# Performance work log

Measured on AMD Instinct MI355X. Metric: run time of the kernel, lower is better.

The kernel has to match this reference:

```python
import jax, jax.numpy as jnp
import numpy as np

N, E = 100000, 800000   # nodes, edges
H, F = 12, 8            # heads, per-head features
D = H * F               # 96 = num_in_features
LRELU_SLOPE = 0.2
LN_EPS = 1e-6


def setup_inputs() -> dict:
    key = jax.random.key(0)
    k1, k2, k3, k4, k5, k6 = jax.random.split(key, 6)
    x = jax.random.normal(k1, (N, D), dtype=jnp.float32)
    edge_index = jax.random.randint(k2, (2, E), 0, N, dtype=jnp.int64)
    # linear_proj: Linear(D, H*F, bias=False); init std = (D*H*F)**-0.5
    w_proj = jax.random.normal(k3, (D, D), dtype=jnp.float32) * (D * H * F) ** -0.5
    score_src = jax.random.normal(k4, (1, H, F), dtype=jnp.float32) * (H * F) ** -0.5
    score_trg = jax.random.normal(k5, (1, H, F), dtype=jnp.float32) * (H * F) ** -0.5
    ln_weight = jnp.ones((D,), dtype=jnp.float32)
    return {"x": x, "edge_index": edge_index, "w_proj": w_proj,
            "score_src": score_src, "score_trg": score_trg, "ln_weight": ln_weight}


def reference(x, edge_index, w_proj, score_src, score_trg, ln_weight):
    # dropout layers are identity (inference mode)
    src = edge_index[0]
    trg = edge_index[1]
    proj = x.reshape(N, H, F)                        # view, no projection (as in source)
    s_src = jnp.sum(proj * score_src, axis=-1)       # [N, H]
    s_trg = jnp.sum(proj * score_trg, axis=-1)       # [N, H]
    # lift to edges + leaky relu
    scores = s_src[src] + s_trg[trg]                 # [E, H]
    scores = jnp.where(scores >= 0, scores, LRELU_SLOPE * scores)
    # neighborhood-aware (segment) softmax over target nodes
    scores = scores - jnp.max(scores)
    exp_scores = jnp.exp(scores)                     # [E, H]
    denom = jax.ops.segment_sum(exp_scores, trg, num_segments=N)  # [N, H]
    attn = exp_scores / (denom[trg] + 1e-16)         # [E, H]
    # weighted aggregation of lifted source features
    weighted = proj[src] * attn[:, :, None]          # [E, H, F]
    agg = jax.ops.segment_sum(weighted, trg, num_segments=N)      # [N, H, F]
    out = agg.reshape(N, H * F)
    # RMS-style LayerNorm (no mean subtraction, weight only)
    var = jnp.mean(jnp.square(out.astype(jnp.float32)), axis=-1, keepdims=True)
    out = ln_weight * (out * jax.lax.rsqrt(var + LN_EPS))
    out = out @ w_proj.T                             # linear_proj, no bias
    return x + out
```

## Files before the change

kernel.cpp:

```cpp
#include <hip/hip_runtime.h>
#include <math.h>

#define NN 100000
#define EE 800000
#define HH 12
#define FF 8
#define DD 96
#define NBLK_SCAN 98
#define WROW 104

typedef __bf16 bf16x8 __attribute__((ext_vector_type(8)));
typedef float  f32x4  __attribute__((ext_vector_type(4)));

static __device__ __forceinline__ unsigned short f2bf(float f) {
    unsigned u = __builtin_bit_cast(unsigned, f);
    u += 0x7fffu + ((u >> 16) & 1u);
    return (unsigned short)(u >> 16);
}
static __device__ __forceinline__ unsigned packbf(float a, float b) {
    return (unsigned)f2bf(a) | ((unsigned)f2bf(b) << 16);
}

__global__ __launch_bounds__(256) void k_scores(
    const float* __restrict__ x, const float* __restrict__ wsrc,
    const float* __restrict__ wtrg, float* __restrict__ s_src,
    float* __restrict__ s_trg, int* __restrict__ counts)
{
    int tid = blockIdx.x * 256 + threadIdx.x;
    if (tid < NN) counts[tid] = 0;
    if (tid >= NN * HH) return;
    int h = tid % HH;
    int n = tid / HH;
    const float4* xp = (const float4*)(x + (size_t)n * DD + h * FF);
    float4 a = xp[0], b = xp[1];
    const float4* s4 = (const float4*)(wsrc + h * FF);
    const float4* t4 = (const float4*)(wtrg + h * FF);
    float4 sa = s4[0], sb = s4[1];
    float4 ta = t4[0], tb = t4[1];
    s_src[tid] = a.x*sa.x + a.y*sa.y + a.z*sa.z + a.w*sa.w
               + b.x*sb.x + b.y*sb.y + b.z*sb.z + b.w*sb.w;
    s_trg[tid] = a.x*ta.x + a.y*ta.y + a.z*ta.z + a.w*ta.w
               + b.x*tb.x + b.y*tb.y + b.z*tb.z + b.w*tb.w;
}

__global__ __launch_bounds__(256) void k_hist(const int* __restrict__ ei,
                                              int* __restrict__ counts)
{
    int e = blockIdx.x * 256 + threadIdx.x;
    if (e >= EE) return;
    int t = ei[EE + e];
    atomicAdd(&counts[t], 1);
}

__global__ __launch_bounds__(256) void k_chunks(const int* __restrict__ counts,
                                                int* __restrict__ chunks)
{
    __shared__ int sd[256];
    int t = threadIdx.x;
    int base = blockIdx.x * 1024 + t * 4;
    int s = 0;
    #pragma unroll
    for (int j = 0; j < 4; ++j) {
        int i = base + j;
        s += (i < NN) ? counts[i] : 0;
    }
    sd[t] = s;
    __syncthreads();
    for (int off = 128; off > 0; off >>= 1) {
        if (t < off) sd[t] += sd[t + off];
        __syncthreads();
    }
    if (t == 0) chunks[blockIdx.x] = sd[0];
}

__global__ __launch_bounds__(256) void k_scan(const int* __restrict__ counts,
                                              const int* __restrict__ chunks,
                                              int* __restrict__ offsets,
                                              int* __restrict__ cursor)
{
    __shared__ int sc[128];
    __shared__ int sd[256];
    int t = threadIdx.x;
    if (t < 128) sc[t] = (t < NBLK_SCAN) ? chunks[t] : 0;
    __syncthreads();
    for (int off = 1; off < 128; off <<= 1) {
        int u = (t < 128 && t >= off) ? sc[t - off] : 0;
        __syncthreads();
        if (t < 128) sc[t] += u;
        __syncthreads();
    }
    int bof = (blockIdx.x == 0) ? 0 : sc[blockIdx.x - 1];

    int base = blockIdx.x * 1024 + t * 4;
    int c[4];
    int s = 0;
    #pragma unroll
    for (int j = 0; j < 4; ++j) {
        int i = base + j;
        c[j] = (i < NN) ? counts[i] : 0;
        s += c[j];
    }
    sd[t] = s;
    __syncthreads();
    for (int off = 1; off < 256; off <<= 1) {
        int u = (t >= off) ? sd[t - off] : 0;
        __syncthreads();
        sd[t] += u;
        __syncthreads();
    }
    int run = bof + ((t == 0) ? 0 : sd[t - 1]);
    #pragma unroll
    for (int j = 0; j < 4; ++j) {
        int i = base + j;
        if (i < NN) { offsets[i] = run; cursor[i] = run; }
        run += c[j];
    }
}

__global__ __launch_bounds__(256) void k_scatter(const int* __restrict__ ei,
                                                 int* __restrict__ cursor,
                                                 int* __restrict__ esrc)
{
    int e = blockIdx.x * 256 + threadIdx.x;
    if (e >= EE) return;
    int s = ei[e];
    int t = ei[EE + e];
    int pos = atomicAdd(&cursor[t], 1);
    esrc[pos] = s;
}

__global__ __launch_bounds__(768) void k_aggout(
    const float* __restrict__ x, const float* __restrict__ s_src,
    const float* __restrict__ s_trg, const int* __restrict__ offsets,
    const int* __restrict__ counts, const int* __restrict__ esrc,
    const float* __restrict__ lnw, const float* __restrict__ w,
    float* __restrict__ out)
{
    __shared__ char lds_raw[(96 + 64) * WROW * 2];
    __shared__ float nsq[64];
    unsigned short* wl = (unsigned short*)lds_raw;
    unsigned short* yl = ((unsigned short*)lds_raw) + 96 * WROW;
    int t    = threadIdx.x;
    int tile = blockIdx.x * 64;
    int nrem = NN - tile;

    if (t < 64) nsq[t] = 0.f;
    #pragma unroll
    for (int i = 0; i < 3; ++i) {
        int lin = t * 4 + i * 3072;
        int r = lin / 96, c = lin - (lin / 96) * 96;
        float4 v = *(const float4*)(w + lin);
        unsigned* p = (unsigned*)(wl + r * WROW + c);
        p[0] = packbf(v.x, v.y); p[1] = packbf(v.z, v.w);
    }
    __syncthreads();

    {
        int ln = t / HH;
        int h  = t - ln * HH;
        int n  = tile + ln;
        bool valid = (n < NN);
        float st = 0.f; int beg = 0, cnt = 0;
        if (valid) {
            st  = s_trg[n * HH + h];
            beg = offsets[n];
            cnt = counts[n];
        }
        float denom = 0.f;
        float4 aa = {0.f, 0.f, 0.f, 0.f};
        float4 ab = {0.f, 0.f, 0.f, 0.f};
        int s_cur = (cnt > 0) ? esrc[beg] : 0;
        for (int k = 0; k < cnt; ++k) {
            int s_nxt = (k + 1 < cnt) ? esrc[beg + k + 1] : 0;
            float sc = s_src[s_cur * HH + h] + st;
            sc = (sc >= 0.f) ? sc : 0.2f * sc;
            float ex = __expf(sc);
            denom += ex;
            const float4* xp = (const float4*)(x + (size_t)s_cur * DD + h * FF);
            float4 a = xp[0], b = xp[1];
            aa.x += a.x * ex; aa.y += a.y * ex; aa.z += a.z * ex; aa.w += a.w * ex;
            ab.x += b.x * ex; ab.y += b.y * ex; ab.z += b.z * ex; ab.w += b.w * ex;
            s_cur = s_nxt;
        }
        float inv = 1.f / (denom + 1e-16f);
        float yp[8];
        yp[0] = aa.x * inv; yp[1] = aa.y * inv; yp[2] = aa.z * inv; yp[3] = aa.w * inv;
        yp[4] = ab.x * inv; yp[5] = ab.y * inv; yp[6] = ab.z * inv; yp[7] = ab.w * inv;
        float ss = 0.f;
        #pragma unroll
        for (int j = 0; j < 8; ++j) ss += yp[j] * yp[j];
        atomicAdd(&nsq[ln], ss);
        __syncthreads();
        float scale = rsqrtf(nsq[ln] * (1.f / 96.f) + 1e-6f);
        const float4* lw = (const float4*)(lnw + h * FF);
        float4 w1 = lw[0], w2 = lw[1];
        unsigned* yo = (unsigned*)(yl + ln * WROW + h * FF);
        yo[0] = packbf(yp[0] * scale * w1.x, yp[1] * scale * w1.y);
        yo[1] = packbf(yp[2] * scale * w1.z, yp[3] * scale * w1.w);
        yo[2] = packbf(yp[4] * scale * w2.x, yp[5] * scale * w2.y);
        yo[3] = packbf(yp[6] * scale * w2.z, yp[7] * scale * w2.w);
    }
    __syncthreads();

    int wv = t >> 6;
    int l  = t & 63;
    int tt0 = wv * 2;
    int rt  = tt0 / 6;
    int ct0 = tt0 - rt * 6;
    int kchunk = (l >> 4) * 8;
    int arow = rt * 16 + (l & 15);
    f32x4 acc0 = {}, acc1 = {};
    #pragma unroll
    for (int s = 0; s < 3; ++s) {
        bf16x8 af = *(const bf16x8*)(yl + arow * WROW + s * 32 + kchunk);
        bf16x8 b0 = *(const bf16x8*)(wl + ((ct0 + 0) * 16 + (l & 15)) * WROW + s * 32 + kchunk);
        bf16x8 b1 = *(const bf16x8*)(wl + ((ct0 + 1) * 16 + (l & 15)) * WROW + s * 32 + kchunk);
        acc0 = __builtin_amdgcn_mfma_f32_16x16x32_bf16(af, b0, acc0, 0, 0, 0);
        acc1 = __builtin_amdgcn_mfma_f32_16x16x32_bf16(af, b1, acc1, 0, 0, 0);
    }
    __syncthreads();

    float* fb = (float*)lds_raw;
    {
        int row = rt * 16 + (l >> 4) * 4;
        int col = ct0 * 16 + (l & 15);
        #pragma unroll
        for (int r = 0; r < 4; ++r) {
            fb[(row + r) * 97 + col]      = acc0[r];
            fb[(row + r) * 97 + col + 16] = acc1[r];
        }
    }
    __syncthreads();
    #pragma unroll
    for (int i = 0; i < 2; ++i) {
        int lin = t * 4 + i * 3072;
        int r = lin / 96, c = lin - (lin / 96) * 96;
        if (r < nrem) {
            float4 xv = *(const float4*)(x + (size_t)tile * DD + lin);
            float4 o;
            o.x = xv.x + fb[r * 97 + c + 0];
            o.y = xv.y + fb[r * 97 + c + 1];
            o.z = xv.z + fb[r * 97 + c + 2];
            o.w = xv.w + fb[r * 97 + c + 3];
            *(float4*)(out + (size_t)tile * DD + lin) = o;
        }
    }
}

extern "C" void kernel_launch(void* const* d_in, const int* in_sizes, int n_in,
                              void* d_out, int out_size, void* d_ws, size_t ws_size,
                              hipStream_t stream)
{
    const float* x    = (const float*)d_in[0];
    const int*   ei   = (const int*)d_in[1];
    const float* wprj = (const float*)d_in[2];
    const float* wsrc = (const float*)d_in[3];
    const float* wtrg = (const float*)d_in[4];
    const float* lnw  = (const float*)d_in[5];
    float* out = (float*)d_out;

    float* s_src  = (float*)d_ws;
    float* s_trg  = s_src + NN * HH;
    int*   counts = (int*)(s_trg + NN * HH);
    int*   offs   = counts + NN;
    int*   cursor = offs + NN;
    int*   chunks = cursor + NN;
    int*   esrc   = chunks + 128;

    k_scores<<<(NN * HH + 255) / 256, 256, 0, stream>>>(x, wsrc, wtrg, s_src, s_trg, counts);
    k_hist<<<(EE + 255) / 256, 256, 0, stream>>>(ei, counts);
    k_chunks<<<NBLK_SCAN, 256, 0, stream>>>(counts, chunks);
    k_scan<<<NBLK_SCAN, 256, 0, stream>>>(counts, chunks, offs, cursor);
    k_scatter<<<(EE + 255) / 256, 256, 0, stream>>>(ei, cursor, esrc);
    k_aggout<<<(NN + 63) / 64, 768, 0, stream>>>(x, s_src, s_trg, offs, counts, esrc, lnw, wprj, out);
}
```

Measured before the change: 269.6 us.

## Gather bf16 copy of node features and replace scatter atomics with histogram ranks

k_scores now also writes a bf16 copy of x, and the edge-aggregation loop gathers 16-byte bf16 rows instead of 32-byte fp32 rows, halving gather traffic in the dominant kernel. The histogram kernel records each edge's atomic return value as a rank, so the scatter kernel computes positions as offset plus rank without a second round of atomics, and the cursor array goes away. The cost is an extra 19 MB bf16 write plus a rank array, and reduced precision in the aggregated features.

```diff
diff --git a/kernel.cpp b/kernel.cpp
--- a/kernel.cpp
+++ b/kernel.cpp
@@ -20,11 +20,18 @@
 static __device__ __forceinline__ unsigned packbf(float a, float b) {
     return (unsigned)f2bf(a) | ((unsigned)f2bf(b) << 16);
 }
+static __device__ __forceinline__ float bflo(unsigned u) {
+    return __builtin_bit_cast(float, u << 16);
+}
+static __device__ __forceinline__ float bfhi(unsigned u) {
+    return __builtin_bit_cast(float, u & 0xffff0000u);
+}
 
 __global__ __launch_bounds__(256) void k_scores(
     const float* __restrict__ x, const float* __restrict__ wsrc,
     const float* __restrict__ wtrg, float* __restrict__ s_src,
-    float* __restrict__ s_trg, int* __restrict__ counts)
+    float* __restrict__ s_trg, int* __restrict__ counts,
+    unsigned short* __restrict__ xb)
 {
     int tid = blockIdx.x * 256 + threadIdx.x;
     if (tid < NN) counts[tid] = 0;
@@ -33,6 +40,9 @@
     int n = tid / HH;
     const float4* xp = (const float4*)(x + (size_t)n * DD + h * FF);
     float4 a = xp[0], b = xp[1];
+    unsigned* xo = (unsigned*)(xb + (size_t)n * DD + h * FF);
+    xo[0] = packbf(a.x, a.y); xo[1] = packbf(a.z, a.w);
+    xo[2] = packbf(b.x, b.y); xo[3] = packbf(b.z, b.w);
     const float4* s4 = (const float4*)(wsrc + h * FF);
     const float4* t4 = (const float4*)(wtrg + h * FF);
     float4 sa = s4[0], sb = s4[1];
@@ -44,12 +54,13 @@
 }
 
 __global__ __launch_bounds__(256) void k_hist(const int* __restrict__ ei,
-                                              int* __restrict__ counts)
+                                              int* __restrict__ counts,
+                                              int* __restrict__ rank)
 {
     int e = blockIdx.x * 256 + threadIdx.x;
     if (e >= EE) return;
     int t = ei[EE + e];
-    atomicAdd(&counts[t], 1);
+    rank[e] = atomicAdd(&counts[t], 1);
 }
 
 __global__ __launch_bounds__(256) void k_chunks(const int* __restrict__ counts,
@@ -75,8 +86,7 @@
 
 __global__ __launch_bounds__(256) void k_scan(const int* __restrict__ counts,
                                               const int* __restrict__ chunks,
-                                              int* __restrict__ offsets,
-                                              int* __restrict__ cursor)
+                                              int* __restrict__ offsets)
 {
     __shared__ int sc[128];
     __shared__ int sd[256];
@@ -112,29 +122,29 @@
     #pragma unroll
     for (int j = 0; j < 4; ++j) {
         int i = base + j;
-        if (i < NN) { offsets[i] = run; cursor[i] = run; }
+        if (i < NN) offsets[i] = run;
         run += c[j];
     }
 }
 
 __global__ __launch_bounds__(256) void k_scatter(const int* __restrict__ ei,
-                                                 int* __restrict__ cursor,
+                                                 const int* __restrict__ offsets,
+                                                 const int* __restrict__ rank,
                                                  int* __restrict__ esrc)
 {
     int e = blockIdx.x * 256 + threadIdx.x;
     if (e >= EE) return;
     int s = ei[e];
     int t = ei[EE + e];
-    int pos = atomicAdd(&cursor[t], 1);
-    esrc[pos] = s;
+    esrc[offsets[t] + rank[e]] = s;
 }
 
 __global__ __launch_bounds__(768) void k_aggout(
-    const float* __restrict__ x, const float* __restrict__ s_src,
-    const float* __restrict__ s_trg, const int* __restrict__ offsets,
-    const int* __restrict__ counts, const int* __restrict__ esrc,
-    const float* __restrict__ lnw, const float* __restrict__ w,
-    float* __restrict__ out)
+    const float* __restrict__ x, const unsigned short* __restrict__ xb,
+    const float* __restrict__ s_src, const float* __restrict__ s_trg,
+    const int* __restrict__ offsets, const int* __restrict__ counts,
+    const int* __restrict__ esrc, const float* __restrict__ lnw,
+    const float* __restrict__ w, float* __restrict__ out)
 {
     __shared__ char lds_raw[(96 + 64) * WROW * 2];
     __shared__ float nsq[64];
@@ -167,8 +177,7 @@
             cnt = counts[n];
         }
         float denom = 0.f;
-        float4 aa = {0.f, 0.f, 0.f, 0.f};
-        float4 ab = {0.f, 0.f, 0.f, 0.f};
+        float acc[8] = {0.f, 0.f, 0.f, 0.f, 0.f, 0.f, 0.f, 0.f};
         int s_cur = (cnt > 0) ? esrc[beg] : 0;
         for (int k = 0; k < cnt; ++k) {
             int s_nxt = (k + 1 < cnt) ? esrc[beg + k + 1] : 0;
@@ -176,16 +185,17 @@
             sc = (sc >= 0.f) ? sc : 0.2f * sc;
             float ex = __expf(sc);
             denom += ex;
-            const float4* xp = (const float4*)(x + (size_t)s_cur * DD + h * FF);
-            float4 a = xp[0], b = xp[1];
-            aa.x += a.x * ex; aa.y += a.y * ex; aa.z += a.z * ex; aa.w += a.w * ex;
-            ab.x += b.x * ex; ab.y += b.y * ex; ab.z += b.z * ex; ab.w += b.w * ex;
+            uint4 q = *(const uint4*)(xb + (size_t)s_cur * DD + h * FF);
+            acc[0] += bflo(q.x) * ex; acc[1] += bfhi(q.x) * ex;
+            acc[2] += bflo(q.y) * ex; acc[3] += bfhi(q.y) * ex;
+            acc[4] += bflo(q.z) * ex; acc[5] += bfhi(q.z) * ex;
+            acc[6] += bflo(q.w) * ex; acc[7] += bfhi(q.w) * ex;
             s_cur = s_nxt;
         }
         float inv = 1.f / (denom + 1e-16f);
         float yp[8];
-        yp[0] = aa.x * inv; yp[1] = aa.y * inv; yp[2] = aa.z * inv; yp[3] = aa.w * inv;
-        yp[4] = ab.x * inv; yp[5] = ab.y * inv; yp[6] = ab.z * inv; yp[7] = ab.w * inv;
+        #pragma unroll
+        for (int j = 0; j < 8; ++j) yp[j] = acc[j] * inv;
         float ss = 0.f;
         #pragma unroll
         for (int j = 0; j < 8; ++j) ss += yp[j] * yp[j];
@@ -263,14 +273,15 @@
     float* s_trg  = s_src + NN * HH;
     int*   counts = (int*)(s_trg + NN * HH);
     int*   offs   = counts + NN;
-    int*   cursor = offs + NN;
-    int*   chunks = cursor + NN;
-    int*   esrc   = chunks + 128;
-
-    k_scores<<<(NN * HH + 255) / 256, 256, 0, stream>>>(x, wsrc, wtrg, s_src, s_trg, counts);
-    k_hist<<<(EE + 255) / 256, 256, 0, stream>>>(ei, counts);
+    int*   chunks = offs + NN;
+    int*   rank   = chunks + 128;
+    int*   esrc   = rank + EE;
+    unsigned short* xb = (unsigned short*)(esrc + EE);
+
+    k_scores<<<(NN * HH + 255) / 256, 256, 0, stream>>>(x, wsrc, wtrg, s_src, s_trg, counts, xb);
+    k_hist<<<(EE + 255) / 256, 256, 0, stream>>>(ei, counts, rank);
     k_chunks<<<NBLK_SCAN, 256, 0, stream>>>(counts, chunks);
-    k_scan<<<NBLK_SCAN, 256, 0, stream>>>(counts, chunks, offs, cursor);
-    k_scatter<<<(EE + 255) / 256, 256, 0, stream>>>(ei, cursor, esrc);
-    k_aggout<<<(NN + 63) / 64, 768, 0, stream>>>(x, s_src, s_trg, offs, counts, esrc, lnw, wprj, out);
-}
+    k_scan<<<NBLK_SCAN, 256, 0, stream>>>(counts, chunks, offs);
+    k_scatter<<<(EE + 255) / 256, 256, 0, stream>>>(ei, offs, rank, esrc);
+    k_aggout<<<(NN + 63) / 64, 768, 0, stream>>>(x, xb, s_src, s_trg, offs, counts, esrc, lnw, wprj, out);
+}
```

New measurement: 221.1 us. -18.0%, faster.
